# Optimization experiments

Hardware: AMD Instinct MI355X
Metric: run time of the kernel (lower is better)

The kernel has to match this reference:

```python
import jax, jax.numpy as jnp
import numpy as np

N = 100000
E = 1600000
D = 128
LAYERS = 2


def setup_inputs() -> dict:
    key = jax.random.key(0)
    k1, k2, k3, k4, k5, k6 = jax.random.split(key, 6)
    features = jax.random.normal(k1, (N, D), dtype=jnp.float32)
    edge_row = jax.random.randint(k2, (E,), 0, N)
    edge_col = jax.random.randint(k3, (E,), 0, N)
    edge_val = jax.random.uniform(k4, (E,), dtype=jnp.float32)
    # new_features[index] = out_features with out_features having N rows =>
    # index is a permutation covering all N nodes
    index = jax.random.permutation(k5, N)
    a_in = jax.random.normal(k6, (3,), dtype=jnp.float32)
    return {"features": features, "edge_row": edge_row, "edge_col": edge_col,
            "edge_val": edge_val, "index": index, "a_in": a_in}


def reference(features, edge_row, edge_col, edge_val, index, a_in):
    n, d = features.shape
    # --- normalize_adj: D^{-1/2} A D^{-1/2} (Mat is constant across layers) ---
    rowsum = jax.ops.segment_sum(edge_val, edge_row, num_segments=n)  # [N]
    d_inv_sqrt = jnp.where(rowsum > 0, rowsum ** -0.5, 0.0)
    vals = d_inv_sqrt[edge_row] * edge_val * d_inv_sqrt[edge_col]      # [E]

    # softmax over first Layers+1 entries of a_in
    a = jax.nn.softmax(a_in[:LAYERS + 1])

    # nodes covered by index keep the SpMM result; others keep old features
    covered = jnp.zeros((n,), dtype=bool).at[index].set(True)

    result = a[0] * features
    h = features
    for j in range(LAYERS):
        # SpMM: out[r] = sum_e vals[e] * h[col[e]] for row[e] == r
        out = jax.ops.segment_sum(vals[:, None] * h[edge_col], edge_row,
                                  num_segments=n)                      # [N, D]
        scattered = jnp.zeros_like(h).at[index].set(out)
        h = jnp.where(covered[:, None], scattered, h)
        result = result + a[j + 1] * h
    return result
```

## Files before the change

kernel.cpp:

```cpp
#include <hip/hip_runtime.h>

#define WPB    4
#define SCAN_B 1024
#define P1B    256
#define BKT_SH 8

__device__ __forceinline__ unsigned bf16rne(float x) {
  unsigned u = __float_as_uint(x);
  return (u + 0x7fffu + ((u >> 16) & 1u)) >> 16;
}
__device__ __forceinline__ float bf_lo(unsigned g) { return __uint_as_float(g << 16); }
__device__ __forceinline__ float bf_hi(unsigned g) { return __uint_as_float(g & 0xffff0000u); }

__global__ void softmax3_k(const float* __restrict__ a_in, float* __restrict__ a) {
  if (threadIdx.x == 0 && blockIdx.x == 0) {
    float x0 = a_in[0], x1 = a_in[1], x2 = a_in[2];
    float m = fmaxf(x0, fmaxf(x1, x2));
    float e0 = expf(x0 - m), e1 = expf(x1 - m), e2 = expf(x2 - m);
    float s = e0 + e1 + e2;
    a[0] = e0 / s; a[1] = e1 / s; a[2] = e2 / s;
  }
}

__global__ void tobf16_k(const float2* __restrict__ f, unsigned* __restrict__ hb, int nw) {
  int i = blockIdx.x * 256 + threadIdx.x;
  if (i < nw) {
    float2 v = f[i];
    hb[i] = bf16rne(v.x) | (bf16rne(v.y) << 16);
  }
}

__global__ void p1_k(const int* __restrict__ row, int* __restrict__ bhist,
                     int E, int C, int NB) {
  extern __shared__ int h[];
  for (int k = threadIdx.x; k < NB; k += 256) h[k] = 0;
  __syncthreads();
  int s = blockIdx.x * C, e = min(E, s + C);
  for (int i = s + threadIdx.x; i < e; i += 256)
    atomicAdd(&h[row[i] >> BKT_SH], 1);
  __syncthreads();
  for (int k = threadIdx.x; k < NB; k += 256)
    bhist[(size_t)k * P1B + blockIdx.x] = h[k];
}

__global__ void scanA_k(const int* __restrict__ cnt, int* __restrict__ incl,
                        int* __restrict__ bsum, int n) {
  __shared__ int tmp[SCAN_B];
  int tid = threadIdx.x;
  int g = blockIdx.x * SCAN_B + tid;
  tmp[tid] = (g < n) ? cnt[g] : 0;
  __syncthreads();
  for (int off = 1; off < SCAN_B; off <<= 1) {
    int t = (tid >= off) ? tmp[tid - off] : 0;
    __syncthreads();
    tmp[tid] += t;
    __syncthreads();
  }
  if (g < n) incl[g] = tmp[tid];
  if (tid == SCAN_B - 1) bsum[blockIdx.x] = tmp[tid];
}

__global__ void scanB_k(int* __restrict__ bsum, int nb) {
  __shared__ int tmp[128];
  int tid = threadIdx.x;
  tmp[tid] = (tid < nb) ? bsum[tid] : 0;
  __syncthreads();
  for (int off = 1; off < 128; off <<= 1) {
    int t = (tid >= off) ? tmp[tid - off] : 0;
    __syncthreads();
    tmp[tid] += t;
    __syncthreads();
  }
  if (tid < nb) bsum[tid] = tmp[tid];
}

__global__ void scanC_k(int* __restrict__ boffs, const int* __restrict__ bhist,
                        const int* __restrict__ bsum, int n) {
  int g = blockIdx.x * SCAN_B + threadIdx.x;
  if (g >= n) return;
  int off = (blockIdx.x > 0) ? bsum[blockIdx.x - 1] : 0;
  boffs[g] = boffs[g] + off - bhist[g];
}

__global__ void p2_k(const int* __restrict__ row, const int* __restrict__ col,
                     const float* __restrict__ val, const int* __restrict__ boffs,
                     int2* __restrict__ bedge, int E, int C, int NB) {
  extern __shared__ int cur[];
  for (int k = threadIdx.x; k < NB; k += 256)
    cur[k] = boffs[(size_t)k * P1B + blockIdx.x];
  __syncthreads();
  int s = blockIdx.x * C, e = min(E, s + C);
  for (int i = s + threadIdx.x; i < e; i += 256) {
    int r = row[i];
    int p = atomicAdd(&cur[r >> BKT_SH], 1);
    bedge[p] = make_int2(((r & 255) << 24) | col[i], __float_as_int(val[i]));
  }
}

__global__ void p3_k(const int2* __restrict__ bedge, const int* __restrict__ boffs,
                     int* __restrict__ row_start, float* __restrict__ rowsum,
                     int2* __restrict__ pairs, int E, int N, int NB) {
  __shared__ int rcnt[256];
  __shared__ float rsum[256];
  __shared__ int rbase[256];
  __shared__ int tmp[256];
  int kb = blockIdx.x, t = threadIdx.x;
  int base = boffs[(size_t)kb * P1B];
  int end  = (kb + 1 < NB) ? boffs[(size_t)(kb + 1) * P1B] : E;
  rcnt[t] = 0; rsum[t] = 0.f;
  __syncthreads();
  for (int i = base + t; i < end; i += 256) {
    int2 p = bedge[i];
    int rlo = ((unsigned)p.x) >> 24;
    atomicAdd(&rcnt[rlo], 1);
    atomicAdd(&rsum[rlo], __int_as_float(p.y));
  }
  __syncthreads();
  int v = rcnt[t];
  tmp[t] = v;
  __syncthreads();
  for (int off = 1; off < 256; off <<= 1) {
    int u = (t >= off) ? tmp[t - off] : 0;
    __syncthreads();
    tmp[t] += u;
    __syncthreads();
  }
  rbase[t] = tmp[t] - v;
  int r = (kb << BKT_SH) + t;
  if (r < N) { row_start[r] = base + rbase[t]; rowsum[r] = rsum[t]; }
  __syncthreads();
  rcnt[t] = rbase[t];
  __syncthreads();
  for (int i = base + t; i < end; i += 256) {
    int2 p = bedge[i];
    int rlo = ((unsigned)p.x) >> 24;
    int pos = base + atomicAdd(&rcnt[rlo], 1);
    pairs[pos] = make_int2(p.x & 0xFFFFFF, p.y);
  }
}

__global__ void dis_k(float* __restrict__ rowsum, int n) {
  int i = blockIdx.x * 256 + threadIdx.x;
  if (i < n) {
    float s = rowsum[i];
    rowsum[i] = (s > 0.0f) ? rsqrtf(s) : 0.0f;
  }
}

__global__ void covered_k(const int* __restrict__ index, int* __restrict__ covered,
                          int* __restrict__ row_start, int E, int n) {
  int i = blockIdx.x * 256 + threadIdx.x;
  if (i == 0) row_start[n] = E;
  if (i < n) covered[index[i]] = 1;
}

__global__ void scale_k(int2* __restrict__ pairs, const float* __restrict__ dis, int E) {
  int i = blockIdx.x * 256 + threadIdx.x;
  if (i < E) {
    int2 p = pairs[i];
    p.y = __float_as_int(__int_as_float(p.y) * dis[p.x]);
    pairs[i] = p;
  }
}

#define SPMM_BODY(HSRC)                                                        \
  float ax0 = 0.f, ay0 = 0.f, ax1 = 0.f, ay1 = 0.f;                            \
  for (int base = beg; base < end; base += 64) {                               \
    int m = end - base; if (m > 64) m = 64;                                    \
    int2 p = make_int2(0, 0);                                                  \
    if (base + lane < end) p = pairs[base + lane];                             \
    int pc = p.x; float pv = __int_as_float(p.y);                              \
    int j = 0;                                                                 \
    for (; j + 4 <= m; j += 4) {                                               \
      int   c0 = __shfl(pc, j),     c1 = __shfl(pc, j + 1);                    \
      int   c2 = __shfl(pc, j + 2), c3 = __shfl(pc, j + 3);                    \
      float v0 = __shfl(pv, j),     v1 = __shfl(pv, j + 1);                    \
      float v2 = __shfl(pv, j + 2), v3 = __shfl(pv, j + 3);                    \
      unsigned g0 = HSRC[(size_t)c0 * 64 + lane];                              \
      unsigned g1 = HSRC[(size_t)c1 * 64 + lane];                              \
      unsigned g2 = HSRC[(size_t)c2 * 64 + lane];                              \
      unsigned g3 = HSRC[(size_t)c3 * 64 + lane];                              \
      ax0 = fmaf(v0, bf_lo(g0), ax0); ay0 = fmaf(v0, bf_hi(g0), ay0);          \
      ax1 = fmaf(v1, bf_lo(g1), ax1); ay1 = fmaf(v1, bf_hi(g1), ay1);          \
      ax0 = fmaf(v2, bf_lo(g2), ax0); ay0 = fmaf(v2, bf_hi(g2), ay0);          \
      ax1 = fmaf(v3, bf_lo(g3), ax1); ay1 = fmaf(v3, bf_hi(g3), ay1);          \
    }                                                                          \
    for (; j < m; ++j) {                                                       \
      int c = __shfl(pc, j); float v = __shfl(pv, j);                          \
      unsigned g = HSRC[(size_t)c * 64 + lane];                                \
      ax0 = fmaf(v, bf_lo(g), ax0); ay0 = fmaf(v, bf_hi(g), ay0);              \
    }                                                                          \
  }

__global__ void spmm1_k(const int* __restrict__ row_start, const int2* __restrict__ pairs,
                        const float* __restrict__ dis, const unsigned* __restrict__ hB,
                        const int* __restrict__ index, unsigned* __restrict__ hA, int n) {
  int wave = blockIdx.x * WPB + (threadIdx.x >> 6);
  if (wave >= n) return;
  int lane = threadIdx.x & 63;
  int beg = row_start[wave], end = row_start[wave + 1];
  SPMM_BODY(hB)
  float dr = dis[wave];
  float x = (ax0 + ax1) * dr, y = (ay0 + ay1) * dr;
  hA[(size_t)index[wave] * 64 + lane] = bf16rne(x) | (bf16rne(y) << 16);
}

__global__ void spmm2_k(const int* __restrict__ row_start, const int2* __restrict__ pairs,
                        const float* __restrict__ dis, const unsigned* __restrict__ hA,
                        const int* __restrict__ index, const float2* __restrict__ feat,
                        float2* __restrict__ out, const float* __restrict__ a, int n) {
  int wave = blockIdx.x * WPB + (threadIdx.x >> 6);
  if (wave >= n) return;
  int lane = threadIdx.x & 63;
  int beg = row_start[wave], end = row_start[wave + 1];
  SPMM_BODY(hA)
  float dr = dis[wave];
  float hx = (ax0 + ax1) * dr, hy = (ay0 + ay1) * dr;
  size_t o = (size_t)index[wave] * 64 + lane;
  unsigned g = hA[o];
  float2 f = feat[o];
  float a0 = a[0], a1 = a[1], a2 = a[2];
  out[o] = make_float2(fmaf(a2, hx, fmaf(a1, bf_lo(g), a0 * f.x)),
                       fmaf(a2, hy, fmaf(a1, bf_hi(g), a0 * f.y)));
}

__global__ void fixup1_k(const int* __restrict__ covered, const unsigned* __restrict__ hB,
                         unsigned* __restrict__ hA, int n) {
  int v = blockIdx.x * 256 + threadIdx.x;
  if (v >= n || covered[v]) return;
  for (int d = 0; d < 64; ++d) hA[(size_t)v * 64 + d] = hB[(size_t)v * 64 + d];
}

__global__ void fixup2_k(const int* __restrict__ covered, const float2* __restrict__ feat,
                         float2* __restrict__ out, const float* __restrict__ a, int n) {
  int v = blockIdx.x * 256 + threadIdx.x;
  if (v >= n || covered[v]) return;
  float s = a[0] + a[1] + a[2];
  for (int d = 0; d < 64; ++d) {
    float2 f = feat[(size_t)v * 64 + d];
    out[(size_t)v * 64 + d] = make_float2(s * f.x, s * f.y);
  }
}

extern "C" void kernel_launch(void* const* d_in, const int* in_sizes, int n_in,
                              void* d_out, int out_size, void* d_ws, size_t ws_size,
                              hipStream_t stream) {
  const float* features = (const float*)d_in[0];
  const int*   edge_row = (const int*)d_in[1];
  const int*   edge_col = (const int*)d_in[2];
  const float* edge_val = (const float*)d_in[3];
  const int*   index    = (const int*)d_in[4];
  const float* a_in     = (const float*)d_in[5];

  const int E = in_sizes[1];
  const int N = in_sizes[4];
  const int NB = (N + 255) >> BKT_SH;
  const int NBH = NB * P1B;
  const int C = (E + P1B - 1) / P1B;

  float* out = (float*)d_out;

  char* ws = (char*)d_ws;
  size_t off = 0;
  auto carve = [&](size_t bytes) -> char* {
    char* p = ws + off;
    off = (off + bytes + 255) & ~(size_t)255;
    return p;
  };
  float* a_buf     = (float*)carve(16 * sizeof(float));
  float* rowsum    = (float*)carve((size_t)N * 4);
  int*   covered   = (int*)carve((size_t)N * 4);
  int*   row_start = (int*)carve((size_t)(N + 1) * 4);
  int*   bsum      = (int*)carve(256 * 4);
  int2*  pairs     = (int2*)carve((size_t)E * 8);
  unsigned* hB     = (unsigned*)carve((size_t)N * 64 * 4);
  size_t ov_bytes = (size_t)NBH * 4 * 2 + (size_t)E * 8 + 1024;
  size_t hA_bytes = (size_t)N * 64 * 4;
  char* ovl = carve(ov_bytes > hA_bytes ? ov_bytes : hA_bytes);
  int*  bhist = (int*)ovl;
  int*  boffs = (int*)(ovl + (((size_t)NBH * 4 + 255) & ~(size_t)255));
  int2* bedge = (int2*)(ovl + 2 * (((size_t)NBH * 4 + 255) & ~(size_t)255));
  unsigned* hA = (unsigned*)ovl;
  (void)ws_size; (void)n_in; (void)out_size;

  const int nbE = (E + 255) / 256;
  const int nbW = (N * 64 + 255) / 256;
  const int nbScan = (NBH + SCAN_B - 1) / SCAN_B;
  const int nbN = (N + 255) / 256;
  const size_t ldsB = (size_t)NB * 4;

  hipMemsetAsync(covered, 0, (size_t)N * 4, stream);
  softmax3_k<<<1, 64, 0, stream>>>(a_in, a_buf);
  tobf16_k<<<nbW, 256, 0, stream>>>((const float2*)features, hB, N * 64);
  p1_k<<<P1B, 256, ldsB, stream>>>(edge_row, bhist, E, C, NB);
  scanA_k<<<nbScan, SCAN_B, 0, stream>>>(bhist, boffs, bsum, NBH);
  scanB_k<<<1, 128, 0, stream>>>(bsum, nbScan);
  scanC_k<<<nbScan, SCAN_B, 0, stream>>>(boffs, bhist, bsum, NBH);
  p2_k<<<P1B, 256, ldsB, stream>>>(edge_row, edge_col, edge_val, boffs, bedge, E, C, NB);
  p3_k<<<NB, 256, 0, stream>>>(bedge, boffs, row_start, rowsum, pairs, E, N, NB);
  dis_k<<<nbN, 256, 0, stream>>>(rowsum, N);
  covered_k<<<nbN, 256, 0, stream>>>(index, covered, row_start, E, N);
  scale_k<<<nbE, 256, 0, stream>>>(pairs, rowsum, E);

  const int nbSpmm = (N + WPB - 1) / WPB;
  spmm1_k<<<nbSpmm, WPB * 64, 0, stream>>>(row_start, pairs, rowsum, hB, index, hA, N);
  fixup1_k<<<nbN, 256, 0, stream>>>(covered, hB, hA, N);
  spmm2_k<<<nbSpmm, WPB * 64, 0, stream>>>(row_start, pairs, rowsum, hA, index,
                                           (const float2*)features, (float2*)out,
                                           a_buf, N);
  fixup2_k<<<nbN, 256, 0, stream>>>(covered, (const float2*)features,
                                    (float2*)out, a_buf, N);
}
```

Before: 235.7 us.

## Split SpMM waves into quarter-wave edge groups with uint4 gathers; fuse prep kernels

The SpMM is remapped so each 16-lane quarter of a wave handles a different edge and loads a whole 128-wide bf16 row as uint4. Each wave now has 16 edges in flight per iteration, and the quarters are combined with cross-lane xor shuffles at the end. This targets gather latency and memory-level parallelism on short rows of about 16 edges. The small setup kernels (softmax, bf16 conversion, covered, row_start tail) are merged into one, and the rsqrt normalisation moves into p3, which cuts launches. spmm2 now reads the a0 term from the bf16 copy of the features instead of fp32, which saves bandwidth but adds rounding error to that term.

```diff
diff --git a/kernel.cpp b/kernel.cpp
--- a/kernel.cpp
+++ b/kernel.cpp
@@ -12,21 +12,23 @@
 __device__ __forceinline__ float bf_lo(unsigned g) { return __uint_as_float(g << 16); }
 __device__ __forceinline__ float bf_hi(unsigned g) { return __uint_as_float(g & 0xffff0000u); }
 
-__global__ void softmax3_k(const float* __restrict__ a_in, float* __restrict__ a) {
-  if (threadIdx.x == 0 && blockIdx.x == 0) {
+__global__ void prep_k(const float2* __restrict__ f, unsigned* __restrict__ hb, int nw,
+                       const float* __restrict__ a_in, float* __restrict__ a_buf,
+                       const int* __restrict__ index, int* __restrict__ covered,
+                       int* __restrict__ row_start, int E, int N) {
+  int i = blockIdx.x * 256 + threadIdx.x;
+  if (i < nw) {
+    float2 v = f[i];
+    hb[i] = bf16rne(v.x) | (bf16rne(v.y) << 16);
+  }
+  if (i < N) covered[index[i]] = 1;
+  if (i == 0) {
+    row_start[N] = E;
     float x0 = a_in[0], x1 = a_in[1], x2 = a_in[2];
     float m = fmaxf(x0, fmaxf(x1, x2));
     float e0 = expf(x0 - m), e1 = expf(x1 - m), e2 = expf(x2 - m);
     float s = e0 + e1 + e2;
-    a[0] = e0 / s; a[1] = e1 / s; a[2] = e2 / s;
-  }
-}
-
-__global__ void tobf16_k(const float2* __restrict__ f, unsigned* __restrict__ hb, int nw) {
-  int i = blockIdx.x * 256 + threadIdx.x;
-  if (i < nw) {
-    float2 v = f[i];
-    hb[i] = bf16rne(v.x) | (bf16rne(v.y) << 16);
+    a_buf[0] = e0 / s; a_buf[1] = e1 / s; a_buf[2] = e2 / s;
   }
 }
 
@@ -98,7 +100,7 @@
 }
 
 __global__ void p3_k(const int2* __restrict__ bedge, const int* __restrict__ boffs,
-                     int* __restrict__ row_start, float* __restrict__ rowsum,
+                     int* __restrict__ row_start, float* __restrict__ dis,
                      int2* __restrict__ pairs, int E, int N, int NB) {
   __shared__ int rcnt[256];
   __shared__ float rsum[256];
@@ -127,7 +129,11 @@
   }
   rbase[t] = tmp[t] - v;
   int r = (kb << BKT_SH) + t;
-  if (r < N) { row_start[r] = base + rbase[t]; rowsum[r] = rsum[t]; }
+  if (r < N) {
+    row_start[r] = base + rbase[t];
+    float s = rsum[t];
+    dis[r] = (s > 0.0f) ? rsqrtf(s) : 0.0f;
+  }
   __syncthreads();
   rcnt[t] = rbase[t];
   __syncthreads();
@@ -137,21 +143,6 @@
     int pos = base + atomicAdd(&rcnt[rlo], 1);
     pairs[pos] = make_int2(p.x & 0xFFFFFF, p.y);
   }
-}
-
-__global__ void dis_k(float* __restrict__ rowsum, int n) {
-  int i = blockIdx.x * 256 + threadIdx.x;
-  if (i < n) {
-    float s = rowsum[i];
-    rowsum[i] = (s > 0.0f) ? rsqrtf(s) : 0.0f;
-  }
-}
-
-__global__ void covered_k(const int* __restrict__ index, int* __restrict__ covered,
-                          int* __restrict__ row_start, int E, int n) {
-  int i = blockIdx.x * 256 + threadIdx.x;
-  if (i == 0) row_start[n] = E;
-  if (i < n) covered[index[i]] = 1;
 }
 
 __global__ void scale_k(int2* __restrict__ pairs, const float* __restrict__ dis, int E) {
@@ -163,72 +154,97 @@
   }
 }
 
-#define SPMM_BODY(HSRC)                                                        \
-  float ax0 = 0.f, ay0 = 0.f, ax1 = 0.f, ay1 = 0.f;                            \
-  for (int base = beg; base < end; base += 64) {                               \
-    int m = end - base; if (m > 64) m = 64;                                    \
-    int2 p = make_int2(0, 0);                                                  \
-    if (base + lane < end) p = pairs[base + lane];                             \
-    int pc = p.x; float pv = __int_as_float(p.y);                              \
-    int j = 0;                                                                 \
-    for (; j + 4 <= m; j += 4) {                                               \
-      int   c0 = __shfl(pc, j),     c1 = __shfl(pc, j + 1);                    \
-      int   c2 = __shfl(pc, j + 2), c3 = __shfl(pc, j + 3);                    \
-      float v0 = __shfl(pv, j),     v1 = __shfl(pv, j + 1);                    \
-      float v2 = __shfl(pv, j + 2), v3 = __shfl(pv, j + 3);                    \
-      unsigned g0 = HSRC[(size_t)c0 * 64 + lane];                              \
-      unsigned g1 = HSRC[(size_t)c1 * 64 + lane];                              \
-      unsigned g2 = HSRC[(size_t)c2 * 64 + lane];                              \
-      unsigned g3 = HSRC[(size_t)c3 * 64 + lane];                              \
-      ax0 = fmaf(v0, bf_lo(g0), ax0); ay0 = fmaf(v0, bf_hi(g0), ay0);          \
-      ax1 = fmaf(v1, bf_lo(g1), ax1); ay1 = fmaf(v1, bf_hi(g1), ay1);          \
-      ax0 = fmaf(v2, bf_lo(g2), ax0); ay0 = fmaf(v2, bf_hi(g2), ay0);          \
-      ax1 = fmaf(v3, bf_lo(g3), ax1); ay1 = fmaf(v3, bf_hi(g3), ay1);          \
-    }                                                                          \
-    for (; j < m; ++j) {                                                       \
-      int c = __shfl(pc, j); float v = __shfl(pv, j);                          \
-      unsigned g = HSRC[(size_t)c * 64 + lane];                                \
-      ax0 = fmaf(v, bf_lo(g), ax0); ay0 = fmaf(v, bf_hi(g), ay0);              \
-    }                                                                          \
-  }
+__device__ __forceinline__ void acc8(float v, uint4 g, float* a) {
+  a[0] = fmaf(v, bf_lo(g.x), a[0]); a[1] = fmaf(v, bf_hi(g.x), a[1]);
+  a[2] = fmaf(v, bf_lo(g.y), a[2]); a[3] = fmaf(v, bf_hi(g.y), a[3]);
+  a[4] = fmaf(v, bf_lo(g.z), a[4]); a[5] = fmaf(v, bf_hi(g.z), a[5]);
+  a[6] = fmaf(v, bf_lo(g.w), a[6]); a[7] = fmaf(v, bf_hi(g.w), a[7]);
+}
+
+__device__ __forceinline__ void spmm_body(const int* __restrict__ row_start,
+                                          const int2* __restrict__ pairs,
+                                          const uint4* __restrict__ h4,
+                                          int wave, int lane, float* a) {
+  int q = lane >> 4, ql = lane & 15;
+  int beg = row_start[wave], end = row_start[wave + 1];
+  for (int base = beg; base < end; base += 64) {
+    int2 p = make_int2(0, 0);
+    if (base + lane < end) p = pairs[base + lane];
+    int pc = p.x; float pv = __int_as_float(p.y);
+    int m = end - base; if (m > 64) m = 64;
+    for (int j = 0; j < m; j += 16) {
+      int   c0 = __shfl(pc, j + q),      c1 = __shfl(pc, j + 4 + q);
+      int   c2 = __shfl(pc, j + 8 + q),  c3 = __shfl(pc, j + 12 + q);
+      float v0 = __shfl(pv, j + q),      v1 = __shfl(pv, j + 4 + q);
+      float v2 = __shfl(pv, j + 8 + q),  v3 = __shfl(pv, j + 12 + q);
+      uint4 g0 = h4[(size_t)c0 * 16 + ql];
+      uint4 g1 = h4[(size_t)c1 * 16 + ql];
+      uint4 g2 = h4[(size_t)c2 * 16 + ql];
+      uint4 g3 = h4[(size_t)c3 * 16 + ql];
+      acc8(v0, g0, a); acc8(v1, g1, a);
+      acc8(v2, g2, a); acc8(v3, g3, a);
+    }
+  }
+#pragma unroll
+  for (int i = 0; i < 8; ++i) a[i] += __shfl_xor(a[i], 16);
+#pragma unroll
+  for (int i = 0; i < 8; ++i) a[i] += __shfl_xor(a[i], 32);
+}
 
 __global__ void spmm1_k(const int* __restrict__ row_start, const int2* __restrict__ pairs,
-                        const float* __restrict__ dis, const unsigned* __restrict__ hB,
-                        const int* __restrict__ index, unsigned* __restrict__ hA, int n) {
+                        const float* __restrict__ dis, const uint4* __restrict__ hB4,
+                        const int* __restrict__ index, uint4* __restrict__ hA4, int n) {
   int wave = blockIdx.x * WPB + (threadIdx.x >> 6);
   if (wave >= n) return;
   int lane = threadIdx.x & 63;
-  int beg = row_start[wave], end = row_start[wave + 1];
-  SPMM_BODY(hB)
-  float dr = dis[wave];
-  float x = (ax0 + ax1) * dr, y = (ay0 + ay1) * dr;
-  hA[(size_t)index[wave] * 64 + lane] = bf16rne(x) | (bf16rne(y) << 16);
+  float a[8] = {0.f, 0.f, 0.f, 0.f, 0.f, 0.f, 0.f, 0.f};
+  spmm_body(row_start, pairs, hB4, wave, lane, a);
+  if ((lane >> 4) == 0) {
+    float dr = dis[wave];
+    uint4 pk;
+    pk.x = bf16rne(a[0] * dr) | (bf16rne(a[1] * dr) << 16);
+    pk.y = bf16rne(a[2] * dr) | (bf16rne(a[3] * dr) << 16);
+    pk.z = bf16rne(a[4] * dr) | (bf16rne(a[5] * dr) << 16);
+    pk.w = bf16rne(a[6] * dr) | (bf16rne(a[7] * dr) << 16);
+    hA4[(size_t)index[wave] * 16 + (lane & 15)] = pk;
+  }
 }
 
 __global__ void spmm2_k(const int* __restrict__ row_start, const int2* __restrict__ pairs,
-                        const float* __restrict__ dis, const unsigned* __restrict__ hA,
-                        const int* __restrict__ index, const float2* __restrict__ feat,
-                        float2* __restrict__ out, const float* __restrict__ a, int n) {
+                        const float* __restrict__ dis, const uint4* __restrict__ hA4,
+                        const uint4* __restrict__ hB4, const int* __restrict__ index,
+                        float4* __restrict__ out4, const float* __restrict__ ac, int n) {
   int wave = blockIdx.x * WPB + (threadIdx.x >> 6);
   if (wave >= n) return;
   int lane = threadIdx.x & 63;
-  int beg = row_start[wave], end = row_start[wave + 1];
-  SPMM_BODY(hA)
-  float dr = dis[wave];
-  float hx = (ax0 + ax1) * dr, hy = (ay0 + ay1) * dr;
-  size_t o = (size_t)index[wave] * 64 + lane;
-  unsigned g = hA[o];
-  float2 f = feat[o];
-  float a0 = a[0], a1 = a[1], a2 = a[2];
-  out[o] = make_float2(fmaf(a2, hx, fmaf(a1, bf_lo(g), a0 * f.x)),
-                       fmaf(a2, hy, fmaf(a1, bf_hi(g), a0 * f.y)));
-}
-
-__global__ void fixup1_k(const int* __restrict__ covered, const unsigned* __restrict__ hB,
-                         unsigned* __restrict__ hA, int n) {
+  float a[8] = {0.f, 0.f, 0.f, 0.f, 0.f, 0.f, 0.f, 0.f};
+  spmm_body(row_start, pairs, hA4, wave, lane, a);
+  if ((lane >> 4) == 0) {
+    int ql = lane & 15;
+    float dr = dis[wave];
+    size_t ro = (size_t)index[wave] * 16 + ql;
+    uint4 ga = hA4[ro];
+    uint4 gb = hB4[ro];
+    float c0 = ac[0], c1 = ac[1], c2 = ac[2];
+    float4 w0, w1;
+    w0.x = fmaf(c2, a[0] * dr, fmaf(c1, bf_lo(ga.x), c0 * bf_lo(gb.x)));
+    w0.y = fmaf(c2, a[1] * dr, fmaf(c1, bf_hi(ga.x), c0 * bf_hi(gb.x)));
+    w0.z = fmaf(c2, a[2] * dr, fmaf(c1, bf_lo(ga.y), c0 * bf_lo(gb.y)));
+    w0.w = fmaf(c2, a[3] * dr, fmaf(c1, bf_hi(ga.y), c0 * bf_hi(gb.y)));
+    w1.x = fmaf(c2, a[4] * dr, fmaf(c1, bf_lo(ga.z), c0 * bf_lo(gb.z)));
+    w1.y = fmaf(c2, a[5] * dr, fmaf(c1, bf_hi(ga.z), c0 * bf_hi(gb.z)));
+    w1.z = fmaf(c2, a[6] * dr, fmaf(c1, bf_lo(ga.w), c0 * bf_lo(gb.w)));
+    w1.w = fmaf(c2, a[7] * dr, fmaf(c1, bf_hi(ga.w), c0 * bf_hi(gb.w)));
+    out4[(size_t)index[wave] * 32 + 2 * ql]     = w0;
+    out4[(size_t)index[wave] * 32 + 2 * ql + 1] = w1;
+  }
+}
+
+__global__ void fixup1_k(const int* __restrict__ covered, const uint4* __restrict__ hB4,
+                         uint4* __restrict__ hA4, int n) {
   int v = blockIdx.x * 256 + threadIdx.x;
   if (v >= n || covered[v]) return;
-  for (int d = 0; d < 64; ++d) hA[(size_t)v * 64 + d] = hB[(size_t)v * 64 + d];
+  for (int d = 0; d < 16; ++d) hA4[(size_t)v * 16 + d] = hB4[(size_t)v * 16 + d];
 }
 
 __global__ void fixup2_k(const int* __restrict__ covered, const float2* __restrict__ feat,
@@ -268,7 +284,7 @@
     return p;
   };
   float* a_buf     = (float*)carve(16 * sizeof(float));
-  float* rowsum    = (float*)carve((size_t)N * 4);
+  float* dis       = (float*)carve((size_t)N * 4);
   int*   covered   = (int*)carve((size_t)N * 4);
   int*   row_start = (int*)carve((size_t)(N + 1) * 4);
   int*   bsum      = (int*)carve(256 * 4);
@@ -290,23 +306,22 @@
   const size_t ldsB = (size_t)NB * 4;
 
   hipMemsetAsync(covered, 0, (size_t)N * 4, stream);
-  softmax3_k<<<1, 64, 0, stream>>>(a_in, a_buf);
-  tobf16_k<<<nbW, 256, 0, stream>>>((const float2*)features, hB, N * 64);
+  prep_k<<<nbW, 256, 0, stream>>>((const float2*)features, hB, N * 64,
+                                  a_in, a_buf, index, covered, row_start, E, N);
   p1_k<<<P1B, 256, ldsB, stream>>>(edge_row, bhist, E, C, NB);
   scanA_k<<<nbScan, SCAN_B, 0, stream>>>(bhist, boffs, bsum, NBH);
   scanB_k<<<1, 128, 0, stream>>>(bsum, nbScan);
   scanC_k<<<nbScan, SCAN_B, 0, stream>>>(boffs, bhist, bsum, NBH);
   p2_k<<<P1B, 256, ldsB, stream>>>(edge_row, edge_col, edge_val, boffs, bedge, E, C, NB);
-  p3_k<<<NB, 256, 0, stream>>>(bedge, boffs, row_start, rowsum, pairs, E, N, NB);
-  dis_k<<<nbN, 256, 0, stream>>>(rowsum, N);
-  covered_k<<<nbN, 256, 0, stream>>>(index, covered, row_start, E, N);
-  scale_k<<<nbE, 256, 0, stream>>>(pairs, rowsum, E);
+  p3_k<<<NB, 256, 0, stream>>>(bedge, boffs, row_start, dis, pairs, E, N, NB);
+  scale_k<<<nbE, 256, 0, stream>>>(pairs, dis, E);
 
   const int nbSpmm = (N + WPB - 1) / WPB;
-  spmm1_k<<<nbSpmm, WPB * 64, 0, stream>>>(row_start, pairs, rowsum, hB, index, hA, N);
-  fixup1_k<<<nbN, 256, 0, stream>>>(covered, hB, hA, N);
-  spmm2_k<<<nbSpmm, WPB * 64, 0, stream>>>(row_start, pairs, rowsum, hA, index,
-                                           (const float2*)features, (float2*)out,
+  spmm1_k<<<nbSpmm, WPB * 64, 0, stream>>>(row_start, pairs, dis, (const uint4*)hB,
+                                           index, (uint4*)hA, N);
+  fixup1_k<<<nbN, 256, 0, stream>>>(covered, (const uint4*)hB, (uint4*)hA, N);
+  spmm2_k<<<nbSpmm, WPB * 64, 0, stream>>>(row_start, pairs, dis, (const uint4*)hA,
+                                           (const uint4*)hB, index, (float4*)out,
                                            a_buf, N);
   fixup2_k<<<nbN, 256, 0, stream>>>(covered, (const float2*)features,
                                     (float2*)out, a_buf, N);
```

Result: faster. 219.0 us (-7.1%).
